# Kernel tuning notes

Hardware: AMD Instinct MI355X
Metric: run time of the kernel (lower is better)

Reference implementation:

```python
import jax, jax.numpy as jnp
import numpy as np

OUTPUT_SIZE = 50000
HIDDEN = 512


def setup_inputs() -> dict:
    key = jax.random.key(0)
    k1, k2, k3, k4 = jax.random.split(key, 4)
    input_value = jax.random.normal(k1, (4, 2048, HIDDEN), dtype=jnp.float32)
    mask_tensor = jax.random.randint(k2, (4, 2048, 32), 0, OUTPUT_SIZE, dtype=jnp.int64)
    weight = jax.random.normal(k3, (OUTPUT_SIZE, HIDDEN), dtype=jnp.float32)
    bias = jax.random.uniform(k4, (OUTPUT_SIZE,), dtype=jnp.float32)
    return {"input_value": input_value, "mask_tensor": mask_tensor,
            "weight": weight, "bias": bias}


def reference(input_value, mask_tensor, weight, bias):
    # gather per-token candidate weights: [b, s, m, h]
    part_weight = weight[mask_tensor]
    # gather per-token candidate biases: [b, s, m]
    part_bias = bias[mask_tensor]
    out = jnp.einsum('bsh,bsmh->bsm', input_value, part_weight) + part_bias
    return jax.nn.relu(out)
```

## Files before the change

kernel.cpp:

```cpp
#include <hip/hip_runtime.h>
#include <hip/hip_bf16.h>

#define HIDDEN 512
#define M_PER_TOKEN 32
#define BUCKET_CAP 32

typedef _Float16 half8 __attribute__((ext_vector_type(8)));
typedef float    f32x4 __attribute__((ext_vector_type(4)));

__global__ __launch_bounds__(256) void prep_kernel(
    const float* __restrict__ input,
    _Float16*    __restrict__ in_h,
    int*         __restrict__ counts,
    int*         __restrict__ padded,
    int n_chunks, int n_rows)
{
    int i = blockIdx.x * 256 + threadIdx.x;
    if (i < n_chunks) {
        const float4 a = ((const float4*)input)[2 * i];
        const float4 b = ((const float4*)input)[2 * i + 1];
        half8 h;
        h[0] = (_Float16)a.x; h[1] = (_Float16)a.y;
        h[2] = (_Float16)a.z; h[3] = (_Float16)a.w;
        h[4] = (_Float16)b.x; h[5] = (_Float16)b.y;
        h[6] = (_Float16)b.z; h[7] = (_Float16)b.w;
        ((half8*)in_h)[i] = h;
    }
    if (i < n_rows) {
        counts[i] = 0;
        *(int4*)(padded + ((size_t)i << 5)) = make_int4(0, 0, 0, 0);
    }
}

__global__ __launch_bounds__(256) void scatter_kernel(
    const int* __restrict__ mask,
    int*       __restrict__ counts,
    int*       __restrict__ padded,
    int n_pairs)
{
    int t    = blockIdx.x * 256 + threadIdx.x;
    int base = t * 4;
    if (base + 3 < n_pairs) {
        const int4 m = *(const int4*)(mask + base);
        int r, slot;
        r = m.x; slot = atomicAdd(&counts[r], 1);
        if (slot < BUCKET_CAP) padded[(r << 5) + slot] = base;
        r = m.y; slot = atomicAdd(&counts[r], 1);
        if (slot < BUCKET_CAP) padded[(r << 5) + slot] = base + 1;
        r = m.z; slot = atomicAdd(&counts[r], 1);
        if (slot < BUCKET_CAP) padded[(r << 5) + slot] = base + 2;
        r = m.w; slot = atomicAdd(&counts[r], 1);
        if (slot < BUCKET_CAP) padded[(r << 5) + slot] = base + 3;
    } else {
        for (int i = base; i < n_pairs; ++i) {
            int r = mask[i];
            int slot = atomicAdd(&counts[r], 1);
            if (slot < BUCKET_CAP) padded[(r << 5) + slot] = i;
        }
    }
}

template <int CTRL>
__device__ __forceinline__ float dpp_add(float v) {
    return v + __int_as_float(__builtin_amdgcn_update_dpp(
        0, __float_as_int(v), CTRL, 0xF, 0xF, true));
}

__device__ __forceinline__ float red16(float v) {
    v = dpp_add<0xB1>(v);
    v = dpp_add<0x4E>(v);
    v = dpp_add<0x141>(v);
    v = dpp_add<0x140>(v);
    return v;
}

__device__ __forceinline__ float dot128(const half8 h, const f32x4 wa,
                                        const f32x4 wb) {
    return (float)h[0]*wa[0] + (float)h[1]*wa[1]
         + (float)h[2]*wa[2] + (float)h[3]*wa[3]
         + (float)h[4]*wb[0] + (float)h[5]*wb[1]
         + (float)h[6]*wb[2] + (float)h[7]*wb[3];
}

__global__ __launch_bounds__(256) void row_ffn_kernel(
    const _Float16* __restrict__ in_h,
    const float*    __restrict__ weight,
    const float*    __restrict__ bias,
    const int*      __restrict__ counts,
    const int*      __restrict__ padded,
    float*          __restrict__ out,
    int n_rows, int blocks_per_xcd)
{
    const int b    = (int)blockIdx.x;
    const int bsw  = (b & 7) * blocks_per_xcd + (b >> 3);
    const int wave = threadIdx.x >> 6;
    const int lane = threadIdx.x & 63;
    const int s    = lane & 15;
    const int q    = lane >> 4;
    const int r    = bsw * 4 + wave;
    if (r >= n_rows) return;

    const int* users = padded + ((size_t)r << 5);

    const int   c_raw = counts[r];
    int         pid_cur = users[q];
    const float bv    = bias[r];

    const float* wbase = weight + (size_t)r * HIDDEN + s * 8;
    f32x4 w[8];
#pragma unroll
    for (int j = 0; j < 4; ++j) {
        w[2*j]   = __builtin_nontemporal_load((const f32x4*)(wbase + j*128));
        w[2*j+1] = __builtin_nontemporal_load((const f32x4*)(wbase + j*128 + 4));
    }

    const _Float16* irow0 = in_h + (size_t)(pid_cur >> 5) * HIDDEN + s * 8;
    half8 h0 = *(const half8*)(irow0);
    half8 h1 = *(const half8*)(irow0 + 128);
    half8 h2 = *(const half8*)(irow0 + 256);
    half8 h3 = *(const half8*)(irow0 + 384);

    const int c = (c_raw > BUCKET_CAP) ? BUCKET_CAP : c_raw;

    int pid_next = 0, pid_next2 = 0;
    half8 n0 = h0, n1 = h1, n2 = h2, n3 = h3;
    if (c > 4) {
        const int g4  = c - 4;
        const int off = (q < g4) ? q : (g4 - 1);
        pid_next = users[4 + off];
        const _Float16* irn = in_h + (size_t)(pid_next >> 5) * HIDDEN + s * 8;
        n0 = *(const half8*)(irn);
        n1 = *(const half8*)(irn + 128);
        n2 = *(const half8*)(irn + 256);
        n3 = *(const half8*)(irn + 384);
    }
    if (c > 8) {
        const int g8  = c - 8;
        const int off = (q < g8) ? q : (g8 - 1);
        pid_next2 = users[8 + off];
    }

    float d = dot128(h0, w[0], w[1]) + dot128(h1, w[2], w[3])
            + dot128(h2, w[4], w[5]) + dot128(h3, w[6], w[7]);
    d = red16(d);
    if (s == 0 && q < c) {
        float v = d + bv;
        out[pid_cur] = v > 0.0f ? v : 0.0f;
    }

    for (int u = 4; u < c; u += 4) {
        const int g = c - u;
        pid_cur = pid_next;
        const half8 c0 = n0, c1 = n1, c2 = n2, c3 = n3;

        if (u + 4 < c) {
            pid_next = pid_next2;
            const _Float16* irn =
                in_h + (size_t)(pid_next >> 5) * HIDDEN + s * 8;
            n0 = *(const half8*)(irn);
            n1 = *(const half8*)(irn + 128);
            n2 = *(const half8*)(irn + 256);
            n3 = *(const half8*)(irn + 384);
            if (u + 8 < c) {
                const int gn  = c - (u + 8);
                const int off = (q < gn) ? q : (gn - 1);
                pid_next2 = users[u + 8 + off];
            }
        }

        float e = dot128(c0, w[0], w[1]) + dot128(c1, w[2], w[3])
                + dot128(c2, w[4], w[5]) + dot128(c3, w[6], w[7]);
        e = red16(e);
        if (s == 0 && q < g) {
            float v = e + bv;
            out[pid_cur] = v > 0.0f ? v : 0.0f;
        }
    }
}

__global__ __launch_bounds__(256) void dynamic_ffn_f32_kernel(
    const float* __restrict__ input,
    const int*   __restrict__ mask,
    const float* __restrict__ weight,
    const float* __restrict__ bias,
    float*       __restrict__ out,
    int n_tokens)
{
    const int token = blockIdx.x;
    if (token >= n_tokens) return;
    const int wave = threadIdx.x >> 6;
    const int lane = threadIdx.x & 63;

    const float* in_row = input + (size_t)token * HIDDEN + lane * 8;
    const float4 x0 = *(const float4*)(in_row);
    const float4 x1 = *(const float4*)(in_row + 4);

    const int* midx = mask + (size_t)token * M_PER_TOKEN + wave * 8;
    float*     orow = out  + (size_t)token * M_PER_TOKEN + wave * 8;

    int idx[8];
#pragma unroll
    for (int j = 0; j < 8; ++j) idx[j] = midx[j];

    float acc[8];
#pragma unroll
    for (int j = 0; j < 8; ++j) {
        const float* w = weight + (size_t)idx[j] * HIDDEN + lane * 8;
        const float4 a = *(const float4*)(w);
        const float4 b = *(const float4*)(w + 4);
        acc[j] = x0.x * a.x + x0.y * a.y + x0.z * a.z + x0.w * a.w
               + x1.x * b.x + x1.y * b.y + x1.z * b.z + x1.w * b.w;
    }
#pragma unroll
    for (int j = 0; j < 8; ++j) {
        float p = acc[j];
#pragma unroll
        for (int off = 32; off > 0; off >>= 1)
            p += __shfl_down(p, off, 64);
        if (lane == 0) {
            float v = p + bias[idx[j]];
            orow[j] = v > 0.0f ? v : 0.0f;
        }
    }
}

extern "C" void kernel_launch(void* const* d_in, const int* in_sizes, int n_in,
                              void* d_out, int out_size, void* d_ws, size_t ws_size,
                              hipStream_t stream) {
    const float* input  = (const float*)d_in[0];
    const int*   mask   = (const int*)  d_in[1];
    const float* weight = (const float*)d_in[2];
    const float* bias   = (const float*)d_in[3];
    float*       out    = (float*)d_out;

    const int n_tokens = in_sizes[0] / HIDDEN;
    const int n_pairs  = in_sizes[1];
    const int n_rows   = in_sizes[2] / HIDDEN;

    const size_t in_h_bytes   = (size_t)in_sizes[0] * sizeof(_Float16);
    const size_t counts_bytes = (size_t)n_rows * sizeof(int);
    const size_t padded_bytes = (size_t)n_rows * BUCKET_CAP * sizeof(int);
    const size_t need = in_h_bytes + counts_bytes + padded_bytes;

    if (ws_size >= need) {
        _Float16* in_h   = (_Float16*)d_ws;
        int*      counts = (int*)((char*)d_ws + in_h_bytes);
        int*      padded = (int*)((char*)d_ws + in_h_bytes + counts_bytes);

        const int n_chunks = in_sizes[0] / 8;
        prep_kernel<<<(n_chunks + 255) / 256, 256, 0, stream>>>(
            input, in_h, counts, padded, n_chunks, n_rows);

        const int sc_threads = (n_pairs + 3) / 4;
        scatter_kernel<<<(sc_threads + 255) / 256, 256, 0, stream>>>(
            mask, counts, padded, n_pairs);

        const int n_wave_rows    = (n_rows + 3) / 4;
        const int blocks_per_xcd = (n_wave_rows + 7) / 8;
        const int grid           = blocks_per_xcd * 8;
        row_ffn_kernel<<<grid, 256, 0, stream>>>(
            in_h, weight, bias, counts, padded, out, n_rows, blocks_per_xcd);
    } else {
        dynamic_ffn_f32_kernel<<<n_tokens, 256, 0, stream>>>(
            input, mask, weight, bias, out, n_tokens);
    }
}
```

Before: 201.2 us.

## Process eight weight rows per wave with next-row state prefetch

Each wave now handles eight consecutive weight rows instead of one. While computing the current row it prefetches the next row's count, bias, weights and first input slice, so per-wave setup cost is amortised and load latency overlaps compute. The inner per-row loop drops the two-deep user prefetch, and the grid shrinks eightfold, which lowers wave-level parallelism. The prep kernel now zeroes the full padded bucket array rather than only its first four entries per row.

```diff
diff --git a/kernel.cpp b/kernel.cpp
--- a/kernel.cpp
+++ b/kernel.cpp
@@ -4,6 +4,7 @@
 #define HIDDEN 512
 #define M_PER_TOKEN 32
 #define BUCKET_CAP 32
+#define RPW 8
 
 typedef _Float16 half8 __attribute__((ext_vector_type(8)));
 typedef float    f32x4 __attribute__((ext_vector_type(4)));
@@ -26,10 +27,8 @@
         h[6] = (_Float16)b.z; h[7] = (_Float16)b.w;
         ((half8*)in_h)[i] = h;
     }
-    if (i < n_rows) {
-        counts[i] = 0;
-        *(int4*)(padded + ((size_t)i << 5)) = make_int4(0, 0, 0, 0);
-    }
+    if (i < n_rows) counts[i] = 0;
+    if (i < n_rows * 8) ((int4*)padded)[i] = make_int4(0, 0, 0, 0);
 }
 
 __global__ __launch_bounds__(256) void scatter_kernel(
@@ -82,6 +81,34 @@
          + (float)h[6]*wb[2] + (float)h[7]*wb[3];
 }
 
+struct RState {
+    int   c;
+    int   pid0;
+    float bv;
+    f32x4 w0, w1, w2, w3, w4, w5, w6, w7;
+};
+
+__device__ __forceinline__ RState issue_state(
+    const float* __restrict__ weight, const float* __restrict__ bias,
+    const int* __restrict__ counts, const int* __restrict__ padded,
+    int r, int s, int q)
+{
+    RState S;
+    S.c    = counts[r];
+    S.pid0 = (padded + ((size_t)r << 5))[q];
+    S.bv   = bias[r];
+    const float* wb = weight + (size_t)r * HIDDEN + s * 8;
+    S.w0 = __builtin_nontemporal_load((const f32x4*)(wb +   0));
+    S.w1 = __builtin_nontemporal_load((const f32x4*)(wb +   4));
+    S.w2 = __builtin_nontemporal_load((const f32x4*)(wb + 128));
+    S.w3 = __builtin_nontemporal_load((const f32x4*)(wb + 132));
+    S.w4 = __builtin_nontemporal_load((const f32x4*)(wb + 256));
+    S.w5 = __builtin_nontemporal_load((const f32x4*)(wb + 260));
+    S.w6 = __builtin_nontemporal_load((const f32x4*)(wb + 384));
+    S.w7 = __builtin_nontemporal_load((const f32x4*)(wb + 388));
+    return S;
+}
+
 __global__ __launch_bounds__(256) void row_ffn_kernel(
     const _Float16* __restrict__ in_h,
     const float*    __restrict__ weight,
@@ -97,84 +124,64 @@
     const int lane = threadIdx.x & 63;
     const int s    = lane & 15;
     const int q    = lane >> 4;
-    const int r    = bsw * 4 + wave;
+    const int wgid = bsw * 4 + wave;
+
+    int r = wgid * RPW;
     if (r >= n_rows) return;
-
-    const int* users = padded + ((size_t)r << 5);
-
-    const int   c_raw = counts[r];
-    int         pid_cur = users[q];
-    const float bv    = bias[r];
-
-    const float* wbase = weight + (size_t)r * HIDDEN + s * 8;
-    f32x4 w[8];
-#pragma unroll
-    for (int j = 0; j < 4; ++j) {
-        w[2*j]   = __builtin_nontemporal_load((const f32x4*)(wbase + j*128));
-        w[2*j+1] = __builtin_nontemporal_load((const f32x4*)(wbase + j*128 + 4));
-    }
-
-    const _Float16* irow0 = in_h + (size_t)(pid_cur >> 5) * HIDDEN + s * 8;
-    half8 h0 = *(const half8*)(irow0);
-    half8 h1 = *(const half8*)(irow0 + 128);
-    half8 h2 = *(const half8*)(irow0 + 256);
-    half8 h3 = *(const half8*)(irow0 + 384);
-
-    const int c = (c_raw > BUCKET_CAP) ? BUCKET_CAP : c_raw;
-
-    int pid_next = 0, pid_next2 = 0;
-    half8 n0 = h0, n1 = h1, n2 = h2, n3 = h3;
-    if (c > 4) {
-        const int g4  = c - 4;
-        const int off = (q < g4) ? q : (g4 - 1);
-        pid_next = users[4 + off];
-        const _Float16* irn = in_h + (size_t)(pid_next >> 5) * HIDDEN + s * 8;
-        n0 = *(const half8*)(irn);
-        n1 = *(const half8*)(irn + 128);
-        n2 = *(const half8*)(irn + 256);
-        n3 = *(const half8*)(irn + 384);
-    }
-    if (c > 8) {
-        const int g8  = c - 8;
-        const int off = (q < g8) ? q : (g8 - 1);
-        pid_next2 = users[8 + off];
-    }
-
-    float d = dot128(h0, w[0], w[1]) + dot128(h1, w[2], w[3])
-            + dot128(h2, w[4], w[5]) + dot128(h3, w[6], w[7]);
-    d = red16(d);
-    if (s == 0 && q < c) {
-        float v = d + bv;
-        out[pid_cur] = v > 0.0f ? v : 0.0f;
-    }
-
-    for (int u = 4; u < c; u += 4) {
-        const int g = c - u;
-        pid_cur = pid_next;
-        const half8 c0 = n0, c1 = n1, c2 = n2, c3 = n3;
-
-        if (u + 4 < c) {
-            pid_next = pid_next2;
-            const _Float16* irn =
-                in_h + (size_t)(pid_next >> 5) * HIDDEN + s * 8;
-            n0 = *(const half8*)(irn);
-            n1 = *(const half8*)(irn + 128);
-            n2 = *(const half8*)(irn + 256);
-            n3 = *(const half8*)(irn + 384);
-            if (u + 8 < c) {
-                const int gn  = c - (u + 8);
-                const int off = (q < gn) ? q : (gn - 1);
-                pid_next2 = users[u + 8 + off];
+    const int r_end = (r + RPW < n_rows) ? r + RPW : n_rows;
+
+    RState S = issue_state(weight, bias, counts, padded, r, s, q);
+    const _Float16* ir0 = in_h + (size_t)(S.pid0 >> 5) * HIDDEN + s * 8;
+    half8 hl0 = *(const half8*)(ir0);
+    half8 hl1 = *(const half8*)(ir0 + 128);
+    half8 hl2 = *(const half8*)(ir0 + 256);
+    half8 hl3 = *(const half8*)(ir0 + 384);
+
+#pragma unroll
+    for (int k = 0; k < RPW; ++k) {
+        const int rn = (r + 1 < r_end) ? r + 1 : r;
+
+        RState SN = issue_state(weight, bias, counts, padded, rn, s, q);
+
+        const int  c     = (S.c > BUCKET_CAP) ? BUCKET_CAP : S.c;
+        const int* users = padded + ((size_t)r << 5);
+        int pidA = (c > 4) ? users[4 + q] : 0;
+
+        float d = dot128(hl0, S.w0, S.w1) + dot128(hl1, S.w2, S.w3)
+                + dot128(hl2, S.w4, S.w5) + dot128(hl3, S.w6, S.w7);
+        d = red16(d);
+        if (s == 0 && q < c) {
+            float v = d + S.bv;
+            out[S.pid0] = v > 0.0f ? v : 0.0f;
+        }
+
+        const _Float16* irn = in_h + (size_t)(SN.pid0 >> 5) * HIDDEN + s * 8;
+        half8 hn0 = *(const half8*)(irn);
+        half8 hn1 = *(const half8*)(irn + 128);
+        half8 hn2 = *(const half8*)(irn + 256);
+        half8 hn3 = *(const half8*)(irn + 384);
+
+        for (int u = 4; u < c; u += 4) {
+            const _Float16* ir = in_h + (size_t)(pidA >> 5) * HIDDEN + s * 8;
+            const half8 a0 = *(const half8*)(ir);
+            const half8 a1 = *(const half8*)(ir + 128);
+            const half8 a2 = *(const half8*)(ir + 256);
+            const half8 a3 = *(const half8*)(ir + 384);
+            const int pidS = pidA;
+            pidA = (u + 4 < c) ? users[u + 4 + q] : 0;
+            float e = dot128(a0, S.w0, S.w1) + dot128(a1, S.w2, S.w3)
+                    + dot128(a2, S.w4, S.w5) + dot128(a3, S.w6, S.w7);
+            e = red16(e);
+            if (s == 0 && q < c - u) {
+                float v = e + S.bv;
+                out[pidS] = v > 0.0f ? v : 0.0f;
             }
         }
 
-        float e = dot128(c0, w[0], w[1]) + dot128(c1, w[2], w[3])
-                + dot128(c2, w[4], w[5]) + dot128(c3, w[6], w[7]);
-        e = red16(e);
-        if (s == 0 && q < g) {
-            float v = e + bv;
-            out[pid_cur] = v > 0.0f ? v : 0.0f;
-        }
+        if (r + 1 >= r_end) break;
+        r = rn;
+        S = SN;
+        hl0 = hn0; hl1 = hn1; hl2 = hn2; hl3 = hn3;
     }
 }
 
@@ -255,8 +262,9 @@
         scatter_kernel<<<(sc_threads + 255) / 256, 256, 0, stream>>>(
             mask, counts, padded, n_pairs);
 
-        const int n_wave_rows    = (n_rows + 3) / 4;
-        const int blocks_per_xcd = (n_wave_rows + 7) / 8;
+        const int n_wave_rows    = (n_rows + RPW - 1) / RPW;
+        const int n_blocks       = (n_wave_rows + 3) / 4;
+        const int blocks_per_xcd = (n_blocks + 7) / 8;
         const int grid           = blocks_per_xcd * 8;
         row_ffn_kernel<<<grid, 256, 0, stream>>>(
             in_h, weight, bias, counts, padded, out, n_rows, blocks_per_xcd);
```

New measurement: 207.3 us. 3.0% more time.
